# Kernel optimization log

Hardware: AMD Instinct MI355X
Metric: run time of the kernel (lower is better)

Reference implementation:

```python
import jax, jax.numpy as jnp
import numpy as np

N_NODES = 100000
N_EDGES = 1000000
D = 64
LN_EPS = 1e-5
DIV_EPS = 1e-6


def _layernorm(x, g, b):
    mu = x.mean(-1, keepdims=True)
    var = ((x - mu) ** 2).mean(-1, keepdims=True)
    return (x - mu) * jax.lax.rsqrt(var + LN_EPS) * g + b


def _linear_params(key, d_in, d_out):
    kw, kb = jax.random.split(key)
    s = 1.0 / np.sqrt(d_in)
    w = jax.random.uniform(kw, (d_in, d_out), jnp.float32, -s, s)
    b = jax.random.uniform(kb, (d_out,), jnp.float32, -s, s)
    return w, b


def setup_inputs() -> dict:
    key = jax.random.key(0)
    ks = jax.random.split(key, 10)
    h = jax.random.normal(ks[0], (N_NODES, D), jnp.float32)
    e = jax.random.normal(ks[1], (N_EDGES, D), jnp.float32)
    src = jax.random.randint(ks[2], (N_EDGES,), 0, N_NODES)
    dst = jax.random.randint(ks[3], (N_EDGES,), 0, N_NODES)
    A1w, A1b = _linear_params(ks[4], D, D)
    A2w, A2b = _linear_params(ks[5], D, D)
    B1w, B1b = _linear_params(ks[6], D, D)
    B2w, B2b = _linear_params(ks[7], D, D)
    B3w, B3b = _linear_params(ks[8], D, D)
    return {
        "h": h, "e": e, "src": src, "dst": dst,
        "A1w": A1w, "A1b": A1b, "A2w": A2w, "A2b": A2b,
        "B1w": B1w, "B1b": B1b, "B2w": B2w, "B2b": B2b,
        "B3w": B3w, "B3b": B3b,
        "ln_e_g": jnp.ones((D,), jnp.float32), "ln_e_b": jnp.zeros((D,), jnp.float32),
        "ln_h_g": jnp.ones((D,), jnp.float32), "ln_h_b": jnp.zeros((D,), jnp.float32),
    }


def reference(h, e, src, dst, A1w, A1b, A2w, A2b, B1w, B1b, B2w, B2b, B3w, B3b,
              ln_e_g, ln_e_b, ln_h_g, ln_h_b):
    # dense projections (small GEMMs, d=64)
    A1h = h @ A1w + A1b          # [N, D]
    A2h = h @ A2w + A2b          # [N, D]
    B1h = h @ B1w + B1b          # [N, D]
    B2h = h @ B2w + B2b          # [N, D]
    B3e = e @ B3w + B3b          # [E, D]

    # apply_edges u_add_v: B1h[src] + B2h[dst], plus B3e
    e_ji = B1h[src] + B2h[dst] + B3e            # [E, D]
    e_ji = jax.nn.relu(_layernorm(e_ji, ln_e_g, ln_e_b))
    e_ji = e_ji + e                              # residual (in==out)

    sigma = jax.nn.sigmoid(e_ji)                 # [E, D]

    # update_all u_mul_e sum: sum over incoming edges at dst of A2h[src]*sigma
    sum_sigma_h = jax.ops.segment_sum(A2h[src] * sigma, dst, num_segments=N_NODES)
    sum_sigma = jax.ops.segment_sum(sigma, dst, num_segments=N_NODES)

    h_forward = sum_sigma_h / (sum_sigma + DIV_EPS)
    h_out = jax.nn.relu(_layernorm(A1h + h_forward, ln_h_g, ln_h_b))
    h_out = h_out + h                            # residual
    return (h_out, e_ji)
```

## Files before the change

### kernel.cpp

```cpp
#include <hip/hip_runtime.h>

#define D 64
#define LN_EPS 1e-5f
#define DIV_EPS 1e-6f

typedef __attribute__((ext_vector_type(8))) short bf16x8;
typedef __attribute__((ext_vector_type(4))) float f32x4;

__device__ __forceinline__ short f2bf(float f) {
  unsigned u = __float_as_uint(f);
  unsigned r = (u + 0x7fffu + ((u >> 16) & 1u)) >> 16;
  return (short)r;
}

__device__ __forceinline__ float wave_sum(float v) {
#pragma unroll
  for (int m = 1; m < 64; m <<= 1) v += __shfl_xor(v, m, 64);
  return v;
}

__device__ __forceinline__ bf16x8 load_bfrag(const float* __restrict__ W,
                                             int s, int n0, int lane) {
  const int c = n0 * 16 + (lane & 15);
  const int k0 = s * 32 + ((lane >> 4) << 3);
  bf16x8 b;
#pragma unroll
  for (int j = 0; j < 8; ++j) b[j] = f2bf(W[(k0 + j) * D + c]);
  return b;
}

__device__ __forceinline__ void load_afrags(const float* __restrict__ X,
                                            size_t r0, int lane, bf16x8& a0,
                                            bf16x8& a1) {
  const int q = lane >> 4, m = lane & 15;
  const float* rb = X + (r0 + m) * D;
  const float4* p0 = (const float4*)(rb + q * 8);
  const float4* p1 = (const float4*)(rb + 32 + q * 8);
  float4 v0 = p0[0], v1 = p0[1], v2 = p1[0], v3 = p1[1];
  a0 = (bf16x8){f2bf(v0.x), f2bf(v0.y), f2bf(v0.z), f2bf(v0.w),
                f2bf(v1.x), f2bf(v1.y), f2bf(v1.z), f2bf(v1.w)};
  a1 = (bf16x8){f2bf(v2.x), f2bf(v2.y), f2bf(v2.z), f2bf(v2.w),
                f2bf(v3.x), f2bf(v3.y), f2bf(v3.z), f2bf(v3.w)};
}

__global__ __launch_bounds__(256, 1) void node_proj_mfma(
    const float* __restrict__ h, const float* __restrict__ W0,
    const float* __restrict__ Bb0, const float* __restrict__ W1,
    const float* __restrict__ Bb1, const float* __restrict__ W2,
    const float* __restrict__ Bb2, const float* __restrict__ W3,
    const float* __restrict__ Bb3, float* __restrict__ o0,
    float* __restrict__ o1, float* __restrict__ o2, float* __restrict__ o3,
    int N) {
  const int lane = threadIdx.x & 63;
  const int q = lane >> 4, m = lane & 15;
  const int wave = blockIdx.x * 4 + (threadIdx.x >> 6);
  const int nw = gridDim.x * 4;
  const float* Ws[4] = {W0, W1, W2, W3};
  const float* Bs[4] = {Bb0, Bb1, Bb2, Bb3};
  float* Os[4] = {o0, o1, o2, o3};
  bf16x8 bf[4][2][4];
  float bias[4][4];
#pragma unroll
  for (int mat = 0; mat < 4; ++mat) {
#pragma unroll
    for (int s = 0; s < 2; ++s)
#pragma unroll
      for (int n0 = 0; n0 < 4; ++n0)
        bf[mat][s][n0] = load_bfrag(Ws[mat], s, n0, lane);
#pragma unroll
    for (int n0 = 0; n0 < 4; ++n0) bias[mat][n0] = Bs[mat][n0 * 16 + m];
  }
  for (int r0 = wave * 16; r0 < N; r0 += nw * 16) {
    bf16x8 a0, a1;
    load_afrags(h, (size_t)r0, lane, a0, a1);
#pragma unroll
    for (int mat = 0; mat < 4; ++mat) {
      f32x4 acc[4];
#pragma unroll
      for (int n0 = 0; n0 < 4; ++n0) {
        acc[n0] = (f32x4){0.f, 0.f, 0.f, 0.f};
        acc[n0] = __builtin_amdgcn_mfma_f32_16x16x32_bf16(a0, bf[mat][0][n0],
                                                          acc[n0], 0, 0, 0);
        acc[n0] = __builtin_amdgcn_mfma_f32_16x16x32_bf16(a1, bf[mat][1][n0],
                                                          acc[n0], 0, 0, 0);
      }
      float* Om = Os[mat];
#pragma unroll
      for (int n0 = 0; n0 < 4; ++n0)
#pragma unroll
        for (int r = 0; r < 4; ++r)
          Om[(size_t)(r0 + q * 4 + r) * D + n0 * 16 + m] =
              acc[n0][r] + bias[mat][n0];
    }
  }
}

__global__ __launch_bounds__(256, 3) void edge_mfma2(
    const float* __restrict__ e, const int* __restrict__ src,
    const int* __restrict__ dst, const float* __restrict__ B1h,
    const float* __restrict__ B2h, const float* __restrict__ A2h,
    const float* __restrict__ W3, const float* __restrict__ B3b,
    const float* __restrict__ g, const float* __restrict__ bta,
    float* __restrict__ eout, float* __restrict__ ssh, float* __restrict__ ss,
    int E) {
  __shared__ float xs[64][65];
  const int lane = threadIdx.x & 63;
  const int q = lane >> 4, m = lane & 15;
  const int wid = threadIdx.x >> 6;
  const int gw = blockIdx.x * 4 + wid;
  const int nw = gridDim.x * 4;
  bf16x8 bf[2][4];
#pragma unroll
  for (int s = 0; s < 2; ++s)
#pragma unroll
    for (int n0 = 0; n0 < 4; ++n0) bf[s][n0] = load_bfrag(W3, s, n0, lane);
  const float bb = B3b[lane], gl = g[lane], bl = bta[lane];
  for (int e0 = gw * 16; e0 < E; e0 += nw * 16) {
    bf16x8 a0, a1;
    load_afrags(e, (size_t)e0, lane, a0, a1);
    f32x4 acc[4];
#pragma unroll
    for (int n0 = 0; n0 < 4; ++n0) {
      acc[n0] = (f32x4){0.f, 0.f, 0.f, 0.f};
      acc[n0] =
          __builtin_amdgcn_mfma_f32_16x16x32_bf16(a0, bf[0][n0], acc[n0], 0, 0, 0);
      acc[n0] =
          __builtin_amdgcn_mfma_f32_16x16x32_bf16(a1, bf[1][n0], acc[n0], 0, 0, 0);
    }
#pragma unroll
    for (int n0 = 0; n0 < 4; ++n0)
#pragma unroll
      for (int r = 0; r < 4; ++r)
        xs[(wid << 4) + (q << 2) + r][(n0 << 4) + m] = acc[n0][r];
    for (int t = 0; t < 16; ++t) {
      const int ej = e0 + t;
      const int sN = src[ej], dN = dst[ej];
      const float x = xs[(wid << 4) + t][lane] + bb +
                      B1h[(size_t)sN * D + lane] + B2h[(size_t)dN * D + lane];
      const float a2v = A2h[(size_t)sN * D + lane];
      const float mu = wave_sum(x) * (1.f / 64.f);
      const float dx = x - mu;
      const float var = wave_sum(dx * dx) * (1.f / 64.f);
      float y = dx * rsqrtf(var + LN_EPS) * gl + bl;
      y = fmaxf(y, 0.f) + e[(size_t)ej * D + lane];
      eout[(size_t)ej * D + lane] = y;
      const float sg = 1.f / (1.f + __expf(-y));
      atomicAdd(&ssh[(size_t)dN * D + lane], a2v * sg);
      atomicAdd(&ss[(size_t)dN * D + lane], sg);
    }
  }
}

__global__ __launch_bounds__(256) void node_out_kernel(
    const float* __restrict__ h, const float* __restrict__ A1h,
    const float* __restrict__ ssh, const float* __restrict__ ss,
    const float* __restrict__ g, const float* __restrict__ bta,
    float* __restrict__ hout, int n) {
  const int lane = threadIdx.x & 63;
  const int wave = blockIdx.x * 4 + (threadIdx.x >> 6);
  const int nw = gridDim.x * 4;
  const float gl = g[lane], bl = bta[lane];
  for (int n0 = wave; n0 < n; n0 += nw) {
    const size_t base = (size_t)n0 * D;
    const float x =
        A1h[base + lane] + ssh[base + lane] / (ss[base + lane] + DIV_EPS);
    const float mu = wave_sum(x) * (1.f / 64.f);
    const float dx = x - mu;
    const float var = wave_sum(dx * dx) * (1.f / 64.f);
    float y = dx * rsqrtf(var + LN_EPS) * gl + bl;
    y = fmaxf(y, 0.f) + h[base + lane];
    hout[base + lane] = y;
  }
}

extern "C" void kernel_launch(void* const* d_in, const int* in_sizes, int n_in,
                              void* d_out, int out_size, void* d_ws,
                              size_t ws_size, hipStream_t stream) {
  const float* h = (const float*)d_in[0];
  const float* e = (const float*)d_in[1];
  const int* src = (const int*)d_in[2];
  const int* dst = (const int*)d_in[3];
  const float* A1w = (const float*)d_in[4];
  const float* A1b = (const float*)d_in[5];
  const float* A2w = (const float*)d_in[6];
  const float* A2b = (const float*)d_in[7];
  const float* B1w = (const float*)d_in[8];
  const float* B1b = (const float*)d_in[9];
  const float* B2w = (const float*)d_in[10];
  const float* B2b = (const float*)d_in[11];
  const float* B3w = (const float*)d_in[12];
  const float* B3b = (const float*)d_in[13];
  const float* ln_e_g = (const float*)d_in[14];
  const float* ln_e_b = (const float*)d_in[15];
  const float* ln_h_g = (const float*)d_in[16];
  const float* ln_h_b = (const float*)d_in[17];

  const int N = in_sizes[0] / D;
  const int E = in_sizes[1] / D;

  float* ws = (float*)d_ws;
  float* A1h = ws;
  float* A2h = ws + (size_t)N * D;
  float* B1h = ws + 2 * (size_t)N * D;
  float* B2h = ws + 3 * (size_t)N * D;
  float* ssh = ws + 4 * (size_t)N * D;
  float* ss = ws + 5 * (size_t)N * D;

  float* hout = (float*)d_out;
  float* eout = (float*)d_out + (size_t)N * D;

  hipMemsetAsync(ssh, 0, 2 * (size_t)N * D * sizeof(float), stream);

  node_proj_mfma<<<1563, 256, 0, stream>>>(h, B1w, B1b, B2w, B2b, A1w, A1b,
                                           A2w, A2b, B1h, B2h, A1h, A2h, N);
  edge_mfma2<<<4096, 256, 0, stream>>>(e, src, dst, B1h, B2h, A2h, B3w, B3b,
                                       ln_e_g, ln_e_b, eout, ssh, ss, E);
  node_out_kernel<<<1024, 256, 0, stream>>>(h, A1h, ssh, ss, ln_h_g, ln_h_b,
                                            hout, N);
}
```

Measured before the change: 930.7 us.

## Process edges directly from MFMA accumulator layout with 16-lane row reductions

The edge kernel no longer stages the B3e projection through shared memory and walks 16 edges serially with full-wave reductions. Each lane now handles 4 columns of 4 edges straight from the MFMA accumulator layout, using 16-lane shuffle reductions for LayerNorm. The e tile is cached in LDS for the residual instead of being re-read from global memory, and loads and stores of streamed data use nontemporal hints. The node output kernel also processes 4 rows per wave with vector loads, and grid sizes change; scattered gathers and atomics now touch 16-column strided segments per row rather than one contiguous 64-float row per instruction.

Result: faster. 865.4 us (-7.0%).

```diff
diff --git a/kernel.cpp b/kernel.cpp
--- a/kernel.cpp
+++ b/kernel.cpp
@@ -13,9 +13,13 @@
   return (short)r;
 }
 
-__device__ __forceinline__ float wave_sum(float v) {
-#pragma unroll
-  for (int m = 1; m < 64; m <<= 1) v += __shfl_xor(v, m, 64);
+__device__ __forceinline__ f32x4 ntld4(const float* p) {
+  return __builtin_nontemporal_load((const f32x4*)p);
+}
+
+__device__ __forceinline__ float gsum16(float v) {
+#pragma unroll
+  for (int m = 1; m < 16; m <<= 1) v += __shfl_xor(v, m, 64);
   return v;
 }
 
@@ -95,7 +99,7 @@
   }
 }
 
-__global__ __launch_bounds__(256, 3) void edge_mfma2(
+__global__ __launch_bounds__(256, 3) void edge_mfma3(
     const float* __restrict__ e, const int* __restrict__ src,
     const int* __restrict__ dst, const float* __restrict__ B1h,
     const float* __restrict__ B2h, const float* __restrict__ A2h,
@@ -103,7 +107,7 @@
     const float* __restrict__ g, const float* __restrict__ bta,
     float* __restrict__ eout, float* __restrict__ ssh, float* __restrict__ ss,
     int E) {
-  __shared__ float xs[64][65];
+  __shared__ float es[4][16][68];
   const int lane = threadIdx.x & 63;
   const int q = lane >> 4, m = lane & 15;
   const int wid = threadIdx.x >> 6;
@@ -114,10 +118,29 @@
   for (int s = 0; s < 2; ++s)
 #pragma unroll
     for (int n0 = 0; n0 < 4; ++n0) bf[s][n0] = load_bfrag(W3, s, n0, lane);
-  const float bb = B3b[lane], gl = g[lane], bl = bta[lane];
+  float bb[4], gl[4], bl[4];
+#pragma unroll
+  for (int k = 0; k < 4; ++k) {
+    const int c = m + 16 * k;
+    bb[k] = B3b[c];
+    gl[k] = g[c];
+    bl[k] = bta[c];
+  }
   for (int e0 = gw * 16; e0 < E; e0 += nw * 16) {
-    bf16x8 a0, a1;
-    load_afrags(e, (size_t)e0, lane, a0, a1);
+    const float* rb = e + (size_t)(e0 + m) * D;
+    f32x4 v0 = ntld4(rb + q * 8);
+    f32x4 v1 = ntld4(rb + q * 8 + 4);
+    f32x4 v2 = ntld4(rb + 32 + q * 8);
+    f32x4 v3 = ntld4(rb + 32 + q * 8 + 4);
+    f32x4* erow = (f32x4*)&es[wid][m][0];
+    erow[q * 2] = v0;
+    erow[q * 2 + 1] = v1;
+    erow[8 + q * 2] = v2;
+    erow[8 + q * 2 + 1] = v3;
+    bf16x8 a0 = (bf16x8){f2bf(v0[0]), f2bf(v0[1]), f2bf(v0[2]), f2bf(v0[3]),
+                         f2bf(v1[0]), f2bf(v1[1]), f2bf(v1[2]), f2bf(v1[3])};
+    bf16x8 a1 = (bf16x8){f2bf(v2[0]), f2bf(v2[1]), f2bf(v2[2]), f2bf(v2[3]),
+                         f2bf(v3[0]), f2bf(v3[1]), f2bf(v3[2]), f2bf(v3[3])};
     f32x4 acc[4];
 #pragma unroll
     for (int n0 = 0; n0 < 4; ++n0) {
@@ -127,49 +150,82 @@
       acc[n0] =
           __builtin_amdgcn_mfma_f32_16x16x32_bf16(a1, bf[1][n0], acc[n0], 0, 0, 0);
     }
-#pragma unroll
-    for (int n0 = 0; n0 < 4; ++n0)
-#pragma unroll
-      for (int r = 0; r < 4; ++r)
-        xs[(wid << 4) + (q << 2) + r][(n0 << 4) + m] = acc[n0][r];
-    for (int t = 0; t < 16; ++t) {
-      const int ej = e0 + t;
-      const int sN = src[ej], dN = dst[ej];
-      const float x = xs[(wid << 4) + t][lane] + bb +
-                      B1h[(size_t)sN * D + lane] + B2h[(size_t)dN * D + lane];
-      const float a2v = A2h[(size_t)sN * D + lane];
-      const float mu = wave_sum(x) * (1.f / 64.f);
-      const float dx = x - mu;
-      const float var = wave_sum(dx * dx) * (1.f / 64.f);
-      float y = dx * rsqrtf(var + LN_EPS) * gl + bl;
-      y = fmaxf(y, 0.f) + e[(size_t)ej * D + lane];
-      eout[(size_t)ej * D + lane] = y;
-      const float sg = 1.f / (1.f + __expf(-y));
-      atomicAdd(&ssh[(size_t)dN * D + lane], a2v * sg);
-      atomicAdd(&ss[(size_t)dN * D + lane], sg);
-    }
-  }
-}
-
-__global__ __launch_bounds__(256) void node_out_kernel(
+    const int sv = src[e0 + m];
+    const int dv = dst[e0 + m];
+#pragma unroll
+    for (int r = 0; r < 4; ++r) {
+      const int tr = q * 4 + r;
+      const int sN = __shfl(sv, tr, 64);
+      const int dN = __shfl(dv, tr, 64);
+      const size_t sb = (size_t)sN * D, db = (size_t)dN * D;
+      float x[4], a2[4], part = 0.f;
+#pragma unroll
+      for (int k = 0; k < 4; ++k) {
+        const int c = m + 16 * k;
+        x[k] = acc[k][r] + bb[k] + B1h[sb + c] + B2h[db + c];
+        a2[k] = A2h[sb + c];
+        part += x[k];
+      }
+      const float mu = gsum16(part) * (1.f / 64.f);
+      float dx[4], vp = 0.f;
+#pragma unroll
+      for (int k = 0; k < 4; ++k) {
+        dx[k] = x[k] - mu;
+        vp += dx[k] * dx[k];
+      }
+      const float rs = rsqrtf(gsum16(vp) * (1.f / 64.f) + LN_EPS);
+      const size_t eb = (size_t)(e0 + tr) * D;
+#pragma unroll
+      for (int k = 0; k < 4; ++k) {
+        const int c = m + 16 * k;
+        float y = fmaxf(dx[k] * rs * gl[k] + bl[k], 0.f) + es[wid][tr][c];
+        __builtin_nontemporal_store(y, eout + eb + c);
+        const float sg = 1.f / (1.f + __expf(-y));
+        atomicAdd(&ssh[db + c], a2[k] * sg);
+        atomicAdd(&ss[db + c], sg);
+      }
+    }
+  }
+}
+
+__global__ __launch_bounds__(256) void node_out2(
     const float* __restrict__ h, const float* __restrict__ A1h,
     const float* __restrict__ ssh, const float* __restrict__ ss,
     const float* __restrict__ g, const float* __restrict__ bta,
     float* __restrict__ hout, int n) {
   const int lane = threadIdx.x & 63;
+  const int q = lane >> 4, m = lane & 15;
   const int wave = blockIdx.x * 4 + (threadIdx.x >> 6);
   const int nw = gridDim.x * 4;
-  const float gl = g[lane], bl = bta[lane];
-  for (int n0 = wave; n0 < n; n0 += nw) {
-    const size_t base = (size_t)n0 * D;
-    const float x =
-        A1h[base + lane] + ssh[base + lane] / (ss[base + lane] + DIV_EPS);
-    const float mu = wave_sum(x) * (1.f / 64.f);
-    const float dx = x - mu;
-    const float var = wave_sum(dx * dx) * (1.f / 64.f);
-    float y = dx * rsqrtf(var + LN_EPS) * gl + bl;
-    y = fmaxf(y, 0.f) + h[base + lane];
-    hout[base + lane] = y;
+  const f32x4 gl = ((const f32x4*)g)[m];
+  const f32x4 bl = ((const f32x4*)bta)[m];
+  for (int n0 = wave * 4; n0 < n; n0 += nw * 4) {
+    const int row = n0 + q;
+    if (row >= n) continue;
+    const size_t base = (size_t)row * D + m * 4;
+    f32x4 a1 = ntld4(A1h + base);
+    f32x4 s1 = ntld4(ssh + base);
+    f32x4 s2 = ntld4(ss + base);
+    f32x4 hv = ntld4(h + base);
+    float x[4], part = 0.f;
+#pragma unroll
+    for (int k = 0; k < 4; ++k) {
+      x[k] = a1[k] + s1[k] / (s2[k] + DIV_EPS);
+      part += x[k];
+    }
+    const float mu = gsum16(part) * (1.f / 64.f);
+    float dx[4], vp = 0.f;
+#pragma unroll
+    for (int k = 0; k < 4; ++k) {
+      dx[k] = x[k] - mu;
+      vp += dx[k] * dx[k];
+    }
+    const float rs = rsqrtf(gsum16(vp) * (1.f / 64.f) + LN_EPS);
+    f32x4 y;
+#pragma unroll
+    for (int k = 0; k < 4; ++k)
+      y[k] = fmaxf(dx[k] * rs * gl[k] + bl[k], 0.f) + hv[k];
+    __builtin_nontemporal_store(y, (f32x4*)(hout + base));
   }
 }
 
@@ -213,8 +269,7 @@
 
   node_proj_mfma<<<1563, 256, 0, stream>>>(h, B1w, B1b, B2w, B2b, A1w, A1b,
                                            A2w, A2b, B1h, B2h, A1h, A2h, N);
-  edge_mfma2<<<4096, 256, 0, stream>>>(e, src, dst, B1h, B2h, A2h, B3w, B3b,
+  edge_mfma3<<<3907, 256, 0, stream>>>(e, src, dst, B1h, B2h, A2h, B3w, B3b,
                                        ln_e_g, ln_e_b, eout, ssh, ss, E);
-  node_out_kernel<<<1024, 256, 0, stream>>>(h, A1h, ssh, ss, ln_h_g, ln_h_b,
-                                            hout, N);
-}
+  node_out2<<<2048, 256, 0, stream>>>(h, A1h, ssh, ss, ln_h_g, ln_h_b, hout, N);
+}
```
